# Kernel optimization log

Hardware: AMD Instinct MI355X
Metric: run time of the kernel (lower is better)

Reference implementation:

```python
import jax, jax.numpy as jnp
import numpy as np

EPS = 1e-5
B, BEAMS, DEPTH, NEXP, D = 2048, 4, 3, 4, 128

def _conv(x, w, b):
    y = jax.lax.conv_general_dilated(x, w, (1, 1), 'VALID',
                                     dimension_numbers=('NCHW', 'OIHW', 'NCHW'))
    return y + b[None, :, None, None]

def _bn(x, g, bt):
    m = jnp.mean(x, axis=(0, 2, 3), keepdims=True)
    v = jnp.var(x, axis=(0, 2, 3), keepdims=True)
    return (x - m) * jax.lax.rsqrt(v + EPS) * g[None, :, None, None] + bt[None, :, None, None]

def _pool(x):
    return jax.lax.reduce_window(x, 0.0, jax.lax.add, (1, 1, 2, 2), (1, 1, 2, 2), 'VALID') * 0.25

def setup_inputs() -> dict:
    key = jax.random.key(0)
    ks = jax.random.split(key, 16)
    s = 0.05
    return {
        'x': jax.random.normal(ks[0], (B, 1, 32, 32), jnp.float32),
        'traj': jax.random.normal(ks[1], (DEPTH, B * BEAMS, NEXP), jnp.float32),
        'score_values': jax.random.uniform(ks[2], (BEAMS, DEPTH), jnp.float32, 0.5, 1.0),
        'c1w': jax.random.normal(ks[3], (32, 1, 3, 3), jnp.float32) * s,
        'c1b': jnp.zeros((32,), jnp.float32),
        'c2w': jax.random.normal(ks[4], (32, 32, 3, 3), jnp.float32) * s,
        'c2b': jnp.zeros((32,), jnp.float32),
        'c3w': jax.random.normal(ks[5], (32, 32, 3, 3), jnp.float32) * s,
        'c3b': jnp.zeros((32,), jnp.float32),
        'g1': jnp.ones((32,), jnp.float32), 'bt1': jnp.zeros((32,), jnp.float32),
        'g2': jnp.ones((32,), jnp.float32), 'bt2': jnp.zeros((32,), jnp.float32),
        'g3': jnp.ones((32,), jnp.float32), 'bt3': jnp.zeros((32,), jnp.float32),
        'We': jax.random.normal(ks[6], (3, D, D), jnp.float32) * s,   # (expert, in, out)
        'be': jax.random.normal(ks[7], (3, D), jnp.float32) * s,
        'Wo': jax.random.normal(ks[8], (10, D), jnp.float32) * s,
        'bo': jnp.zeros((10,), jnp.float32),
    }

def reference(x, traj, score_values, c1w, c1b, c2w, c2b, c3w, c3b,
              g1, bt1, g2, bt2, g3, bt3, We, be, Wo, bo):
    h = _pool(jax.nn.relu(_bn(_conv(x, c1w, c1b), g1, bt1)))
    h = _pool(jax.nn.relu(_bn(_conv(h, c2w, c2b), g2, bt2)))
    h = _pool(jax.nn.relu(_bn(_conv(h, c3w, c3b), g3, bt3)))
    feat = h.reshape(B, -1)                                   # [B, 128]
    hs = jnp.broadcast_to(feat[:, None, :], (B, BEAMS, D)).reshape(B * BEAMS, D)
    for step in range(DEPTH):
        idx = jnp.argmax(traj[step], axis=-1)                  # [N] in 0..3
        lin = jnp.einsum('nd,edh->neh', hs, We) + be[None]     # [N, 3, 128]
        all_out = jnp.concatenate([lin, hs[:, None, :]], axis=1)  # expert 3 = Identity
        hs = jax.nn.relu(jnp.take_along_axis(all_out, idx[:, None, None], axis=1)[:, 0])
    preds = hs @ Wo.T + bo                                     # [N, 10]
    return preds * jnp.prod(score_values)
```

## Files before the change

### kernel.cpp

```cpp
#include <hip/hip_runtime.h>
#include <hip/hip_bf16.h>

#define EPSV 1e-5f
typedef __hip_bfloat16 bf16;
typedef __attribute__((ext_vector_type(8))) short v8s;
typedef __attribute__((ext_vector_type(4))) float v4f;
__device__ __forceinline__ float b2f(bf16 v) { return __bfloat162float(v); }
__device__ __forceinline__ bf16 f2b(float v) { return __float2bfloat16(v); }
__device__ __forceinline__ float bs2f(short s) {
  return __uint_as_float(((unsigned)(unsigned short)s) << 16);
}
__device__ __forceinline__ short f2bs(float v) {
  bf16 b = __float2bfloat16(v);
  return *(short*)&b;
}

__global__ __launch_bounds__(256) void fill_k(float* __restrict__ out, float val, int n)
{
  int i = blockIdx.x * 256 + threadIdx.x;
  if (i < n) out[i] = val;
}

__global__ __launch_bounds__(256) void setup_k(
    const float* __restrict__ w2, const float* __restrict__ w3,
    const float* __restrict__ We, const float* __restrict__ Wo,
    bf16* __restrict__ w2b, bf16* __restrict__ w3b,
    bf16* __restrict__ Web, bf16* __restrict__ Wob,
    int* __restrict__ cnt27, float* __restrict__ Macc,
    float* __restrict__ Sacc2, float* __restrict__ Sacc3)
{
  int i = blockIdx.x * 256 + threadIdx.x;
  if (i < 64) cnt27[i] = 0;
  if (i < 512) {
    Macc[i] = 0.f;
    Sacc2[i] = 0.f;
    Sacc3[i] = 0.f;
  }
  if (i < 9216) {
    int oc = i / 288, r = i - oc * 288, s = r >> 5, ic = r & 31;
    w2b[i] = f2b(w2[oc * 288 + ic * 9 + s]);
  } else if (i < 18432) {
    int j = i - 9216;
    int oc = j / 288, r = j - oc * 288, s = r >> 5, ic = r & 31;
    w3b[j] = f2b(w3[oc * 288 + ic * 9 + s]);
  } else if (i < 18432 + 49152) {
    Web[i - 18432] = f2b(We[i - 18432]);
  } else if (i < 18432 + 49152 + 2048) {
    int j = i - 18432 - 49152;
    int k = j >> 4, o = j & 15;
    Wob[j] = (o < 10) ? f2b(Wo[o * 128 + k]) : f2b(0.f);
  }
}

__global__ __launch_bounds__(256) void front_k(
    const float* __restrict__ traj, const float* __restrict__ x,
    int* __restrict__ cnt27, int* __restrict__ lists, float* __restrict__ Macc)
{
  int t = threadIdx.x;
  if (blockIdx.x < 32) {
    int row = blockIdx.x * 256 + t;
    __shared__ int lcnt[64], lbase[64];
    if (t < 64) lcnt[t] = 0;
    __syncthreads();
    int e[3];
#pragma unroll
    for (int s = 0; s < 3; ++s) {
      float4 tv = ((const float4*)traj)[s * 8192 + row];
      int ee = 0; float bv = tv.x;
      if (tv.y > bv) { bv = tv.y; ee = 1; }
      if (tv.z > bv) { bv = tv.z; ee = 2; }
      if (tv.w > bv) { bv = tv.w; ee = 3; }
      e[s] = ee;
    }
    int sig = e[0] + 4 * e[1] + 16 * e[2];
    int my = atomicAdd(&lcnt[sig], 1);
    __syncthreads();
    if (t < 64) lbase[t] = atomicAdd(&cnt27[t], lcnt[t]);
    __syncthreads();
    lists[sig * 8192 + lbase[sig] + my] = row;
    return;
  }
  int blk = blockIdx.x - 32;
  __shared__ __align__(16) float xs[1024];
  float M[45], S[9];
#pragma unroll
  for (int k = 0; k < 45; ++k) M[k] = 0.f;
#pragma unroll
  for (int k = 0; k < 9; ++k) S[k] = 0.f;
  for (int im = 0; im < 4; ++im) {
    int img = blk * 4 + im;
    ((float4*)xs)[t] = ((const float4*)(x + img * 1024))[t];
    __syncthreads();
    for (int p = t; p < 900; p += 256) {
      int y = p / 30, xx = p - y * 30;
      const float* r0 = xs + y * 32 + xx;
      float v[9];
      v[0] = r0[0];  v[1] = r0[1];  v[2] = r0[2];
      v[3] = r0[32]; v[4] = r0[33]; v[5] = r0[34];
      v[6] = r0[64]; v[7] = r0[65]; v[8] = r0[66];
      int idx = 0;
#pragma unroll
      for (int i = 0; i < 9; ++i) {
        S[i] += v[i];
#pragma unroll
        for (int j = i; j < 9; ++j) M[idx++] = fmaf(v[i], v[j], M[idx]);
      }
    }
    __syncthreads();
  }
  float a[54];
#pragma unroll
  for (int k = 0; k < 45; ++k) a[k] = M[k];
#pragma unroll
  for (int k = 0; k < 9; ++k) a[45 + k] = S[k];
#pragma unroll
  for (int k = 0; k < 54; ++k) {
#pragma unroll
    for (int off = 32; off; off >>= 1) a[k] += __shfl_down(a[k], off, 64);
  }
  __shared__ float red[4][54];
  int wv = t >> 6, lane = t & 63;
  if (lane == 0) {
#pragma unroll
    for (int k = 0; k < 54; ++k) red[wv][k] = a[k];
  }
  __syncthreads();
  if (t < 54)
    atomicAdd(&Macc[(blk & 7) * 64 + t], red[0][t] + red[1][t] + red[2][t] + red[3][t]);
}

__global__ __launch_bounds__(512, 4) void conv12_k(
    const float* __restrict__ x, const float* __restrict__ w1,
    const float* __restrict__ b1, const float* __restrict__ g1,
    const float* __restrict__ bt1, const float* __restrict__ Macc,
    const bf16* __restrict__ w2b, bf16* __restrict__ conv2out,
    float* __restrict__ Sacc2)
{
  int img = blockIdx.x, t = threadIdx.x;
  __shared__ __align__(16) float xs[1024];
  __shared__ float Ms[54], scs[32], shs[32];
  __shared__ short plds[225 * 40];
  __shared__ __align__(16) short w2l[32 * 296];
  __shared__ float red[8][32][2];
  if (t < 256) ((float4*)xs)[t] = ((const float4*)(x + img * 1024))[t];
  {
    const int* w2i = (const int*)w2b;
    int* w2li = (int*)w2l;
#pragma unroll
    for (int k = 0; k < 9; ++k) {
      int i = k * 512 + t;
      int row = i / 144, col = i - row * 144;
      w2li[row * 148 + col] = w2i[i];
    }
  }
  if (t >= 256 && t < 310) {
    int k = t - 256;
    float s = 0.f;
#pragma unroll
    for (int sl = 0; sl < 8; ++sl) s += Macc[sl * 64 + k];
    Ms[k] = s;
  }
  __syncthreads();
  if (t < 32) {
    float w[9];
#pragma unroll
    for (int j = 0; j < 9; ++j) w[j] = w1[t * 9 + j];
    float bias = b1[t];
    float wS = 0.f;
#pragma unroll
    for (int i = 0; i < 9; ++i) wS = fmaf(w[i], Ms[45 + i], wS);
    float wMw = 0.f;
    int idx = 0;
#pragma unroll
    for (int i = 0; i < 9; ++i)
#pragma unroll
      for (int j = i; j < 9; ++j) {
        float coef = (i == j) ? 1.f : 2.f;
        wMw = fmaf(coef * w[i] * w[j], Ms[idx], wMw);
        ++idx;
      }
    const float Np = 2048.f * 900.f;
    float mean = (wS + Np * bias) / Np;
    float sumsq = wMw + 2.f * bias * wS + Np * bias * bias;
    float var = sumsq / Np - mean * mean;
    float sc = g1[t] / sqrtf(var + EPSV);
    scs[t] = sc;
    shs[t] = bt1[t] - mean * sc;
  }
  __syncthreads();
  {
    int ch = t & 31, pg = t >> 5;
    if (pg < 15) {
      float w[9];
#pragma unroll
      for (int j = 0; j < 9; ++j) w[j] = w1[ch * 9 + j];
      float bias = b1[ch], sc = scs[ch], sh = shs[ch];
      const float* rp = xs + 2 * pg * 32;
      float2 l0 = *(const float2*)(rp);
      float2 l1 = *(const float2*)(rp + 32);
      float2 l2 = *(const float2*)(rp + 64);
      float2 l3 = *(const float2*)(rp + 96);
      float a0 = l0.x, b0 = l0.y, a1 = l1.x, b1v = l1.y;
      float a2 = l2.x, b2 = l2.y, a3 = l3.x, b3 = l3.y;
      short* orow = plds + pg * 15 * 40 + ch;
#pragma unroll
      for (int px = 0; px < 15; ++px) {
        int xb = 2 * px;
        float2 p0v = *(const float2*)(rp + xb + 2);
        float2 p1v = *(const float2*)(rp + xb + 34);
        float2 p2v = *(const float2*)(rp + xb + 66);
        float2 p3v = *(const float2*)(rp + xb + 98);
        float e0 = p0v.x, f0 = p0v.y, e1 = p1v.x, f1 = p1v.y;
        float e2 = p2v.x, f2 = p2v.y, e3 = p3v.x, f3 = p3v.y;
        float v00 = bias, v01 = bias, v10 = bias, v11 = bias;
        v00 = fmaf(a0, w[0], v00); v00 = fmaf(b0, w[1], v00); v00 = fmaf(e0, w[2], v00);
        v00 = fmaf(a1, w[3], v00); v00 = fmaf(b1v, w[4], v00); v00 = fmaf(e1, w[5], v00);
        v00 = fmaf(a2, w[6], v00); v00 = fmaf(b2, w[7], v00); v00 = fmaf(e2, w[8], v00);
        v01 = fmaf(b0, w[0], v01); v01 = fmaf(e0, w[1], v01); v01 = fmaf(f0, w[2], v01);
        v01 = fmaf(b1v, w[3], v01); v01 = fmaf(e1, w[4], v01); v01 = fmaf(f1, w[5], v01);
        v01 = fmaf(b2, w[6], v01); v01 = fmaf(e2, w[7], v01); v01 = fmaf(f2, w[8], v01);
        v10 = fmaf(a1, w[0], v10); v10 = fmaf(b1v, w[1], v10); v10 = fmaf(e1, w[2], v10);
        v10 = fmaf(a2, w[3], v10); v10 = fmaf(b2, w[4], v10); v10 = fmaf(e2, w[5], v10);
        v10 = fmaf(a3, w[6], v10); v10 = fmaf(b3, w[7], v10); v10 = fmaf(e3, w[8], v10);
        v11 = fmaf(b1v, w[0], v11); v11 = fmaf(e1, w[1], v11); v11 = fmaf(f1, w[2], v11);
        v11 = fmaf(b2, w[3], v11); v11 = fmaf(e2, w[4], v11); v11 = fmaf(f2, w[5], v11);
        v11 = fmaf(b3, w[6], v11); v11 = fmaf(e3, w[7], v11); v11 = fmaf(f3, w[8], v11);
        float r = fmaxf(fmaf(v00, sc, sh), 0.f) + fmaxf(fmaf(v01, sc, sh), 0.f)
                + fmaxf(fmaf(v10, sc, sh), 0.f) + fmaxf(fmaf(v11, sc, sh), 0.f);
        orow[px * 40] = f2bs(r * 0.25f);
        a0 = e0; a1 = e1; a2 = e2; a3 = e3;
        b0 = f0; b1v = f1; b2 = f2; b3 = f3;
      }
    }
  }
  __syncthreads();
  int lane = t & 63, wv = t >> 6;
  int m = lane & 15, kg = lane >> 4;
  const short* bp0 = w2l + m * 296 + kg * 8;
  const short* bp1 = w2l + (16 + m) * 296 + kg * 8;
  float rs0 = 0.f, rss0 = 0.f, rs1 = 0.f, rss1 = 0.f;
  for (int tile = wv; tile < 11; tile += 8) {
    int pix = tile * 16 + m;
    int cpix = pix < 169 ? pix : 168;
    int y = cpix / 13, xcol = cpix - y * 13;
    const short* ap = plds + (y * 15 + xcol) * 40 + kg * 8;
    v4f acc0 = {0.f, 0.f, 0.f, 0.f}, acc1 = {0.f, 0.f, 0.f, 0.f};
#pragma unroll
    for (int ky = 0; ky < 3; ++ky)
#pragma unroll
      for (int kx = 0; kx < 3; ++kx) {
        int s = ky * 3 + kx;
        v8s a = *(const v8s*)(ap + (ky * 15 + kx) * 40);
        v8s b0 = *(const v8s*)(bp0 + s * 32);
        v8s b1 = *(const v8s*)(bp1 + s * 32);
        acc0 = __builtin_amdgcn_mfma_f32_16x16x32_bf16(a, b0, acc0, 0, 0, 0);
        acc1 = __builtin_amdgcn_mfma_f32_16x16x32_bf16(a, b1, acc1, 0, 0, 0);
      }
#pragma unroll
    for (int j = 0; j < 4; ++j) {
      int pr = tile * 16 + kg * 4 + j;
      if (pr < 169) {
        rs0 += acc0[j]; rss0 = fmaf(acc0[j], acc0[j], rss0);
        rs1 += acc1[j]; rss1 = fmaf(acc1[j], acc1[j], rss1);
        unsigned base = (img * 169 + pr) * 32;
        conv2out[base + m] = f2b(acc0[j]);
        conv2out[base + 16 + m] = f2b(acc1[j]);
      }
    }
  }
  rs0 += __shfl_xor(rs0, 16, 64);  rss0 += __shfl_xor(rss0, 16, 64);
  rs0 += __shfl_xor(rs0, 32, 64);  rss0 += __shfl_xor(rss0, 32, 64);
  rs1 += __shfl_xor(rs1, 16, 64);  rss1 += __shfl_xor(rss1, 16, 64);
  rs1 += __shfl_xor(rs1, 32, 64);  rss1 += __shfl_xor(rss1, 32, 64);
  if (lane < 16) {
    red[wv][lane][0] = rs0;      red[wv][lane][1] = rss0;
    red[wv][16 + lane][0] = rs1; red[wv][16 + lane][1] = rss1;
  }
  __syncthreads();
  if (t < 64) {
    int cc = t >> 1, j = t & 1;
    float s = 0.f;
#pragma unroll
    for (int w8 = 0; w8 < 8; ++w8) s += red[w8][cc][j];
    atomicAdd(&Sacc2[(img & 7) * 64 + t], s);
  }
}

__global__ __launch_bounds__(256, 2) void conv3_mfma_k(
    const bf16* __restrict__ conv2out, const bf16* __restrict__ w3b,
    const float* __restrict__ Sacc2, const float* __restrict__ g2,
    const float* __restrict__ bt2, float* __restrict__ conv3out,
    float* __restrict__ Sacc3)
{
  int t = threadIdx.x, lane = t & 63, wv = t >> 6;
  int m = lane & 15, kg = lane >> 4;
  __shared__ float lsc[32], lsh[32];
  __shared__ short plds[4][36 * 40];
  __shared__ float red[4][32][2];
  if (t < 32) {
    const float invn = 1.f / (2048.f * 169.f);
    float s = 0.f, ssum = 0.f;
#pragma unroll
    for (int sl = 0; sl < 8; ++sl) {
      s += Sacc2[sl * 64 + 2 * t];
      ssum += Sacc2[sl * 64 + 2 * t + 1];
    }
    float mean = s * invn;
    float var = ssum * invn - mean * mean;
    float sc = g2[t] / sqrtf(var + EPSV);
    lsc[t] = sc;
    lsh[t] = bt2[t] - mean * sc;
  }
  __syncthreads();
  int img = blockIdx.x * 4 + wv;
#pragma unroll
  for (int k = 0; k < 18; ++k) {
    int e = k * 64 + lane;
    int pp = e >> 5, c = e & 31;
    int py = pp / 6, px = pp - py * 6;
    int ip0 = (2 * py) * 13 + 2 * px;
    const bf16* bp = conv2out + (img * 169 + ip0) * 32 + c;
    float sc = lsc[c], sh = lsh[c];
    float v = fmaxf(fmaf(b2f(bp[0]), sc, sh), 0.f)
            + fmaxf(fmaf(b2f(bp[32]), sc, sh), 0.f)
            + fmaxf(fmaf(b2f(bp[13 * 32]), sc, sh), 0.f)
            + fmaxf(fmaf(b2f(bp[14 * 32]), sc, sh), 0.f);
    plds[wv][pp * 40 + c] = f2bs(v * 0.25f);
  }
  const short* wbs = (const short*)w3b;
  v8s bfr[9][2];
#pragma unroll
  for (int s = 0; s < 9; ++s)
#pragma unroll
    for (int ob = 0; ob < 2; ++ob)
      bfr[s][ob] = *(const v8s*)(wbs + (ob * 16 + m) * 288 + s * 32 + kg * 8);

  int y = m >> 2, xcol = m & 3;
  const short* ap = plds[wv] + (y * 6 + xcol) * 40 + kg * 8;
  v4f acc0 = {0.f, 0.f, 0.f, 0.f}, acc1 = {0.f, 0.f, 0.f, 0.f};
#pragma unroll
  for (int ky = 0; ky < 3; ++ky)
#pragma unroll
    for (int kx = 0; kx < 3; ++kx) {
      v8s a = *(const v8s*)(ap + (ky * 6 + kx) * 40);
      acc0 = __builtin_amdgcn_mfma_f32_16x16x32_bf16(a, bfr[ky * 3 + kx][0], acc0, 0, 0, 0);
      acc1 = __builtin_amdgcn_mfma_f32_16x16x32_bf16(a, bfr[ky * 3 + kx][1], acc1, 0, 0, 0);
    }
  float rs0 = 0.f, rss0 = 0.f, rs1 = 0.f, rss1 = 0.f;
#pragma unroll
  for (int j = 0; j < 4; ++j) {
    rs0 += acc0[j]; rss0 = fmaf(acc0[j], acc0[j], rss0);
    rs1 += acc1[j]; rss1 = fmaf(acc1[j], acc1[j], rss1);
    int pr = kg * 4 + j;
    unsigned base = (img * 16 + pr) * 32;
    float* o = conv3out;
    o[base + m] = acc0[j];
    o[base + 16 + m] = acc1[j];
  }
  rs0 += __shfl_xor(rs0, 16, 64);  rss0 += __shfl_xor(rss0, 16, 64);
  rs0 += __shfl_xor(rs0, 32, 64);  rss0 += __shfl_xor(rss0, 32, 64);
  rs1 += __shfl_xor(rs1, 16, 64);  rss1 += __shfl_xor(rss1, 16, 64);
  rs1 += __shfl_xor(rs1, 32, 64);  rss1 += __shfl_xor(rss1, 32, 64);
  if (lane < 16) {
    red[wv][lane][0] = rs0;      red[wv][lane][1] = rss0;
    red[wv][16 + lane][0] = rs1; red[wv][16 + lane][1] = rss1;
  }
  __syncthreads();
  if (t < 64) {
    int cc = t >> 1, j = t & 1;
    atomicAdd(&Sacc3[(blockIdx.x & 7) * 64 + t],
              red[0][cc][j] + red[1][cc][j] + red[2][cc][j] + red[3][cc][j]);
  }
}

__global__ __launch_bounds__(256) void moe_fused_k(
    const float* __restrict__ conv3out, const float* __restrict__ Sacc3,
    const float* __restrict__ g3, const float* __restrict__ bt3,
    const bf16* __restrict__ Web, const float* __restrict__ be,
    const bf16* __restrict__ Wob, const float* __restrict__ bo,
    const float* __restrict__ sv, const int* __restrict__ cnt27,
    const int* __restrict__ lists, float* __restrict__ out)
{
  int t = threadIdx.x, lane = t & 63, wv = t >> 6;
  int m = lane & 15, kg = lane >> 4;
  __shared__ float st[4][16][132];
  __shared__ int scnt[64], stile[64];
  __shared__ float lsc[32], lsh[32];

  if (t < 32) {
    const float invn = 1.f / (2048.f * 16.f);
    float s = 0.f, ssum = 0.f;
#pragma unroll
    for (int sl = 0; sl < 8; ++sl) {
      s += Sacc3[sl * 64 + 2 * t];
      ssum += Sacc3[sl * 64 + 2 * t + 1];
    }
    float mean = s * invn;
    float var = ssum * invn - mean * mean;
    float sc = g3[t] / sqrtf(var + EPSV);
    lsc[t] = sc;
    lsh[t] = bt3[t] - mean * sc;
  }
  if (t >= 64 && t < 128) scnt[t - 64] = cnt27[t - 64];
  __syncthreads();
  if (t == 0) {
    int b = 0;
#pragma unroll
    for (int s = 0; s < 64; ++s) { stile[s] = b; b += (scnt[s] + 15) >> 4; }
  }
  __syncthreads();

  int g = blockIdx.x * 4 + wv;
  int sig = -1, tile = 0, cntS = 0;
#pragma unroll
  for (int s = 0; s < 64; ++s) {
    int nt = (scnt[s] + 15) >> 4;
    if (g >= stile[s] && g < stile[s] + nt) { sig = s; tile = g - stile[s]; cntS = scnt[s]; }
  }
  if (sig < 0) return;
  const int* lp = lists + sig * 8192;
  int ra = tile * 16 + m;
  int rowA = lp[ra < cntS ? ra : cntS - 1];

  {
    int img = rowA >> 2;
    const float* cbase = conv3out + img * 512 + kg * 8;
#pragma unroll
    for (int q4 = 0; q4 < 8; ++q4) {
      int c = kg * 8 + q4;
      const float* cp = cbase + q4;
      float sc = lsc[c], sh = lsh[c];
      float r[16];
#pragma unroll
      for (int p = 0; p < 16; ++p)
        r[p] = fmaxf(fmaf(cp[p * 32], sc, sh), 0.f);
      st[wv][m][kg * 32 + q4 * 4 + 0] = (r[0] + r[1] + r[4] + r[5]) * 0.25f;
      st[wv][m][kg * 32 + q4 * 4 + 1] = (r[2] + r[3] + r[6] + r[7]) * 0.25f;
      st[wv][m][kg * 32 + q4 * 4 + 2] = (r[8] + r[9] + r[12] + r[13]) * 0.25f;
      st[wv][m][kg * 32 + q4 * 4 + 3] = (r[10] + r[11] + r[14] + r[15]) * 0.25f;
    }
  }

  int es[3] = { sig & 3, (sig >> 2) & 3, sig >> 4 };
#pragma unroll
  for (int stp = 0; stp < 3; ++stp) {
    int e = es[stp];
    if (e == 3) continue;
    const short* wbs = (const short*)(Web + e * 16384);
    v8s afr[4];
#pragma unroll
    for (int kk = 0; kk < 4; ++kk) {
      float4 a0 = *(const float4*)&st[wv][m][kk * 32 + kg * 8];
      float4 a1 = *(const float4*)&st[wv][m][kk * 32 + kg * 8 + 4];
      afr[kk][0] = f2bs(a0.x); afr[kk][1] = f2bs(a0.y);
      afr[kk][2] = f2bs(a0.z); afr[kk][3] = f2bs(a0.w);
      afr[kk][4] = f2bs(a1.x); afr[kk][5] = f2bs(a1.y);
      afr[kk][6] = f2bs(a1.z); afr[kk][7] = f2bs(a1.w);
    }
#pragma unroll
    for (int ob = 0; ob < 8; ++ob) {
      v4f acc = {0.f, 0.f, 0.f, 0.f};
#pragma unroll
      for (int kk = 0; kk < 4; ++kk) {
        v8s bfr;
#pragma unroll
        for (int j = 0; j < 8; ++j)
          bfr[j] = wbs[(kk * 32 + kg * 8 + j) * 128 + ob * 16 + m];
        acc = __builtin_amdgcn_mfma_f32_16x16x32_bf16(afr[kk], bfr, acc, 0, 0, 0);
      }
      float bb = be[e * 128 + ob * 16 + m];
#pragma unroll
      for (int j = 0; j < 4; ++j)
        st[wv][kg * 4 + j][ob * 16 + m] = fmaxf(acc[j] + bb, 0.f);
    }
  }

  float ps = 1.f;
#pragma unroll
  for (int i = 0; i < 12; ++i) ps *= sv[i];
  const short* wos = (const short*)Wob;
  v8s afr[4];
#pragma unroll
  for (int kk = 0; kk < 4; ++kk) {
    float4 a0 = *(const float4*)&st[wv][m][kk * 32 + kg * 8];
    float4 a1 = *(const float4*)&st[wv][m][kk * 32 + kg * 8 + 4];
    afr[kk][0] = f2bs(a0.x); afr[kk][1] = f2bs(a0.y);
    afr[kk][2] = f2bs(a0.z); afr[kk][3] = f2bs(a0.w);
    afr[kk][4] = f2bs(a1.x); afr[kk][5] = f2bs(a1.y);
    afr[kk][6] = f2bs(a1.z); afr[kk][7] = f2bs(a1.w);
  }
  v4f acc = {0.f, 0.f, 0.f, 0.f};
#pragma unroll
  for (int kk = 0; kk < 4; ++kk) {
    v8s bfr;
#pragma unroll
    for (int j = 0; j < 8; ++j)
      bfr[j] = wos[(kk * 32 + kg * 8 + j) * 16 + m];
    acc = __builtin_amdgcn_mfma_f32_16x16x32_bf16(afr[kk], bfr, acc, 0, 0, 0);
  }
  if (m < 10) {
    float bov = bo[m];
#pragma unroll
    for (int j = 0; j < 4; ++j) {
      int idx = tile * 16 + kg * 4 + j;
      if (idx < cntS) out[lp[idx] * 10 + m] = (acc[j] + bov) * ps;
    }
  }
}

extern "C" void kernel_launch(void* const* d_in, const int* in_sizes, int n_in,
                              void* d_out, int out_size, void* d_ws, size_t ws_size,
                              hipStream_t stream)
{
  float* out = (float*)d_out;

  static const int EXP[19] = {2097152, 98304, 12, 288, 32, 9216, 32, 9216, 32,
                              32, 32, 32, 32, 32, 32, 49152, 384, 1280, 10};
  int bad = -1;
  if (n_in != 19) bad = 100;
  else
    for (int i = 0; i < 19; ++i)
      if (in_sizes[i] != EXP[i]) { bad = i; break; }
  if (bad >= 0) {
    fill_k<<<(out_size + 255) / 256, 256, 0, stream>>>(out, 1000.f + 10.f * bad, out_size);
    return;
  }
  const size_t NEED = 75771904;
  if (ws_size < NEED) {
    fill_k<<<(out_size + 255) / 256, 256, 0, stream>>>(
        out, 3000.f + (float)(ws_size >> 20), out_size);
    return;
  }

  const float* x    = (const float*)d_in[0];
  const float* traj = (const float*)d_in[1];
  const float* sv   = (const float*)d_in[2];
  const float* c1w  = (const float*)d_in[3];
  const float* c1b  = (const float*)d_in[4];
  const float* c2w  = (const float*)d_in[5];
  const float* c3w  = (const float*)d_in[7];
  const float* g1   = (const float*)d_in[9];
  const float* bt1  = (const float*)d_in[10];
  const float* g2   = (const float*)d_in[11];
  const float* bt2  = (const float*)d_in[12];
  const float* g3   = (const float*)d_in[13];
  const float* bt3  = (const float*)d_in[14];
  const float* We   = (const float*)d_in[15];
  const float* be   = (const float*)d_in[16];
  const float* Wo   = (const float*)d_in[17];
  const float* bo   = (const float*)d_in[18];

  char* w = (char*)d_ws;
  bf16*  conv2out = (bf16*)(w + 29491200);
  bf16*  Web      = (bf16*)(w + 56360960);
  float* conv3out = (float*)(w + 61079552);
  float* hsB      = (float*)(w + 69468160);
  float* Macc     = (float*)(w + 73662464);
  float* Sacc2    = (float*)(w + 73664512);
  float* Sacc3    = (float*)(w + 73666560);
  int*   cnt27    = (int*)(w + 73668608);
  bf16*  Wob      = (bf16*)(w + 73670656);
  int*   lists    = (int*)(w + 73674752);
  bf16*  w2b      = (bf16*)hsB;
  bf16*  w3b      = w2b + 9216;

  setup_k<<<272, 256, 0, stream>>>(c2w, c3w, We, Wo, w2b, w3b, Web, Wob,
                                   cnt27, Macc, Sacc2, Sacc3);
  front_k<<<544, 256, 0, stream>>>(traj, x, cnt27, lists, Macc);
  conv12_k<<<2048, 512, 0, stream>>>(x, c1w, c1b, g1, bt1, Macc, w2b, conv2out, Sacc2);
  conv3_mfma_k<<<512, 256, 0, stream>>>(conv2out, w3b, Sacc2, g2, bt2, conv3out, Sacc3);
  moe_fused_k<<<256, 256, 0, stream>>>(conv3out, Sacc3, g3, bt3, Web, be, Wob, bo,
                                       sv, cnt27, lists, out);
}
```

Measured before the change: 92.75 us.

## Warp-specialize conv12 into producer/consumer pipeline over four images per block

Each block of conv12 now processes four images instead of one, and its eight waves are split into two roles. Waves 0-3 compute conv1+BN+ReLU+pool for image i into a double-buffered LDS tile, while waves 4-7 run the MFMA conv2 on image i-1. This amortizes the per-block setup (loading w2 into LDS, computing BN1 statistics) over four images and overlaps the scalar conv1 work with the matrix-core conv2 work. In exchange, shared memory roughly doubles, the grid shrinks to 512 blocks, and each role now has half the waves available for its stage.

Result: faster. 87.42 us, median of 2 (-5.7%).

```diff
diff --git a/kernel.cpp b/kernel.cpp
--- a/kernel.cpp
+++ b/kernel.cpp
@@ -136,13 +136,13 @@
     const bf16* __restrict__ w2b, bf16* __restrict__ conv2out,
     float* __restrict__ Sacc2)
 {
-  int img = blockIdx.x, t = threadIdx.x;
-  __shared__ __align__(16) float xs[1024];
+  int t = threadIdx.x, lane = t & 63, wv = t >> 6;
+  int m = lane & 15, kg = lane >> 4;
+  __shared__ __align__(16) float xs[2][1024];
   __shared__ float Ms[54], scs[32], shs[32];
-  __shared__ short plds[225 * 40];
+  __shared__ short plds[2][225 * 40];
   __shared__ __align__(16) short w2l[32 * 296];
-  __shared__ float red[8][32][2];
-  if (t < 256) ((float4*)xs)[t] = ((const float4*)(x + img * 1024))[t];
+  __shared__ float red[4][32][2];
   {
     const int* w2i = (const int*)w2b;
     int* w2li = (int*)w2l;
@@ -153,12 +153,11 @@
       w2li[row * 148 + col] = w2i[i];
     }
   }
-  if (t >= 256 && t < 310) {
-    int k = t - 256;
+  if (t < 54) {
     float s = 0.f;
 #pragma unroll
-    for (int sl = 0; sl < 8; ++sl) s += Macc[sl * 64 + k];
-    Ms[k] = s;
+    for (int sl = 0; sl < 8; ++sl) s += Macc[sl * 64 + t];
+    Ms[t] = s;
   }
   __syncthreads();
   if (t < 32) {
@@ -188,101 +187,111 @@
     shs[t] = bt1[t] - mean * sc;
   }
   __syncthreads();
-  {
-    int ch = t & 31, pg = t >> 5;
-    if (pg < 15) {
+
+  int img0 = blockIdx.x * 4;
+  float rs0 = 0.f, rss0 = 0.f, rs1 = 0.f, rss1 = 0.f;
+
+  for (int it = 0; it <= 4; ++it) {
+    if (wv < 4 && it < 4)
+      ((float4*)xs[it & 1])[t] = ((const float4*)(x + (img0 + it) * 1024))[t];
+    __syncthreads();
+    if (wv < 4 && it < 4) {
+      int ch = t & 31, rg = t >> 5;
       float w[9];
 #pragma unroll
       for (int j = 0; j < 9; ++j) w[j] = w1[ch * 9 + j];
       float bias = b1[ch], sc = scs[ch], sh = shs[ch];
-      const float* rp = xs + 2 * pg * 32;
-      float2 l0 = *(const float2*)(rp);
-      float2 l1 = *(const float2*)(rp + 32);
-      float2 l2 = *(const float2*)(rp + 64);
-      float2 l3 = *(const float2*)(rp + 96);
-      float a0 = l0.x, b0 = l0.y, a1 = l1.x, b1v = l1.y;
-      float a2 = l2.x, b2 = l2.y, a3 = l3.x, b3 = l3.y;
-      short* orow = plds + pg * 15 * 40 + ch;
-#pragma unroll
-      for (int px = 0; px < 15; ++px) {
-        int xb = 2 * px;
-        float2 p0v = *(const float2*)(rp + xb + 2);
-        float2 p1v = *(const float2*)(rp + xb + 34);
-        float2 p2v = *(const float2*)(rp + xb + 66);
-        float2 p3v = *(const float2*)(rp + xb + 98);
-        float e0 = p0v.x, f0 = p0v.y, e1 = p1v.x, f1 = p1v.y;
-        float e2 = p2v.x, f2 = p2v.y, e3 = p3v.x, f3 = p3v.y;
-        float v00 = bias, v01 = bias, v10 = bias, v11 = bias;
-        v00 = fmaf(a0, w[0], v00); v00 = fmaf(b0, w[1], v00); v00 = fmaf(e0, w[2], v00);
-        v00 = fmaf(a1, w[3], v00); v00 = fmaf(b1v, w[4], v00); v00 = fmaf(e1, w[5], v00);
-        v00 = fmaf(a2, w[6], v00); v00 = fmaf(b2, w[7], v00); v00 = fmaf(e2, w[8], v00);
-        v01 = fmaf(b0, w[0], v01); v01 = fmaf(e0, w[1], v01); v01 = fmaf(f0, w[2], v01);
-        v01 = fmaf(b1v, w[3], v01); v01 = fmaf(e1, w[4], v01); v01 = fmaf(f1, w[5], v01);
-        v01 = fmaf(b2, w[6], v01); v01 = fmaf(e2, w[7], v01); v01 = fmaf(f2, w[8], v01);
-        v10 = fmaf(a1, w[0], v10); v10 = fmaf(b1v, w[1], v10); v10 = fmaf(e1, w[2], v10);
-        v10 = fmaf(a2, w[3], v10); v10 = fmaf(b2, w[4], v10); v10 = fmaf(e2, w[5], v10);
-        v10 = fmaf(a3, w[6], v10); v10 = fmaf(b3, w[7], v10); v10 = fmaf(e3, w[8], v10);
-        v11 = fmaf(b1v, w[0], v11); v11 = fmaf(e1, w[1], v11); v11 = fmaf(f1, w[2], v11);
-        v11 = fmaf(b2, w[3], v11); v11 = fmaf(e2, w[4], v11); v11 = fmaf(f2, w[5], v11);
-        v11 = fmaf(b3, w[6], v11); v11 = fmaf(e3, w[7], v11); v11 = fmaf(f3, w[8], v11);
-        float r = fmaxf(fmaf(v00, sc, sh), 0.f) + fmaxf(fmaf(v01, sc, sh), 0.f)
-                + fmaxf(fmaf(v10, sc, sh), 0.f) + fmaxf(fmaf(v11, sc, sh), 0.f);
-        orow[px * 40] = f2bs(r * 0.25f);
-        a0 = e0; a1 = e1; a2 = e2; a3 = e3;
-        b0 = f0; b1v = f1; b2 = f2; b3 = f3;
+      const float* xb = xs[it & 1];
+      short* pbase = plds[it & 1];
+      for (int rr = rg; rr < 15; rr += 8) {
+        const float* rp = xb + 2 * rr * 32;
+        float2 l0 = *(const float2*)(rp);
+        float2 l1 = *(const float2*)(rp + 32);
+        float2 l2 = *(const float2*)(rp + 64);
+        float2 l3 = *(const float2*)(rp + 96);
+        float a0 = l0.x, b0 = l0.y, a1 = l1.x, b1v = l1.y;
+        float a2 = l2.x, b2 = l2.y, a3 = l3.x, b3 = l3.y;
+        short* orow = pbase + rr * 15 * 40 + ch;
+#pragma unroll
+        for (int px = 0; px < 15; ++px) {
+          int xb2 = 2 * px;
+          float2 p0v = *(const float2*)(rp + xb2 + 2);
+          float2 p1v = *(const float2*)(rp + xb2 + 34);
+          float2 p2v = *(const float2*)(rp + xb2 + 66);
+          float2 p3v = *(const float2*)(rp + xb2 + 98);
+          float e0 = p0v.x, f0 = p0v.y, e1 = p1v.x, f1 = p1v.y;
+          float e2 = p2v.x, f2 = p2v.y, e3 = p3v.x, f3 = p3v.y;
+          float v00 = bias, v01 = bias, v10 = bias, v11 = bias;
+          v00 = fmaf(a0, w[0], v00); v00 = fmaf(b0, w[1], v00); v00 = fmaf(e0, w[2], v00);
+          v00 = fmaf(a1, w[3], v00); v00 = fmaf(b1v, w[4], v00); v00 = fmaf(e1, w[5], v00);
+          v00 = fmaf(a2, w[6], v00); v00 = fmaf(b2, w[7], v00); v00 = fmaf(e2, w[8], v00);
+          v01 = fmaf(b0, w[0], v01); v01 = fmaf(e0, w[1], v01); v01 = fmaf(f0, w[2], v01);
+          v01 = fmaf(b1v, w[3], v01); v01 = fmaf(e1, w[4], v01); v01 = fmaf(f1, w[5], v01);
+          v01 = fmaf(b2, w[6], v01); v01 = fmaf(e2, w[7], v01); v01 = fmaf(f2, w[8], v01);
+          v10 = fmaf(a1, w[0], v10); v10 = fmaf(b1v, w[1], v10); v10 = fmaf(e1, w[2], v10);
+          v10 = fmaf(a2, w[3], v10); v10 = fmaf(b2, w[4], v10); v10 = fmaf(e2, w[5], v10);
+          v10 = fmaf(a3, w[6], v10); v10 = fmaf(b3, w[7], v10); v10 = fmaf(e3, w[8], v10);
+          v11 = fmaf(b1v, w[0], v11); v11 = fmaf(e1, w[1], v11); v11 = fmaf(f1, w[2], v11);
+          v11 = fmaf(b2, w[3], v11); v11 = fmaf(e2, w[4], v11); v11 = fmaf(f2, w[5], v11);
+          v11 = fmaf(b3, w[6], v11); v11 = fmaf(e3, w[7], v11); v11 = fmaf(f3, w[8], v11);
+          float r = fmaxf(fmaf(v00, sc, sh), 0.f) + fmaxf(fmaf(v01, sc, sh), 0.f)
+                  + fmaxf(fmaf(v10, sc, sh), 0.f) + fmaxf(fmaf(v11, sc, sh), 0.f);
+          orow[px * 40] = f2bs(r * 0.25f);
+          a0 = e0; a1 = e1; a2 = e2; a3 = e3;
+          b0 = f0; b1v = f1; b2 = f2; b3 = f3;
+        }
       }
-    }
-  }
-  __syncthreads();
-  int lane = t & 63, wv = t >> 6;
-  int m = lane & 15, kg = lane >> 4;
-  const short* bp0 = w2l + m * 296 + kg * 8;
-  const short* bp1 = w2l + (16 + m) * 296 + kg * 8;
-  float rs0 = 0.f, rss0 = 0.f, rs1 = 0.f, rss1 = 0.f;
-  for (int tile = wv; tile < 11; tile += 8) {
-    int pix = tile * 16 + m;
-    int cpix = pix < 169 ? pix : 168;
-    int y = cpix / 13, xcol = cpix - y * 13;
-    const short* ap = plds + (y * 15 + xcol) * 40 + kg * 8;
-    v4f acc0 = {0.f, 0.f, 0.f, 0.f}, acc1 = {0.f, 0.f, 0.f, 0.f};
-#pragma unroll
-    for (int ky = 0; ky < 3; ++ky)
-#pragma unroll
-      for (int kx = 0; kx < 3; ++kx) {
-        int s = ky * 3 + kx;
-        v8s a = *(const v8s*)(ap + (ky * 15 + kx) * 40);
-        v8s b0 = *(const v8s*)(bp0 + s * 32);
-        v8s b1 = *(const v8s*)(bp1 + s * 32);
-        acc0 = __builtin_amdgcn_mfma_f32_16x16x32_bf16(a, b0, acc0, 0, 0, 0);
-        acc1 = __builtin_amdgcn_mfma_f32_16x16x32_bf16(a, b1, acc1, 0, 0, 0);
+    } else if (wv >= 4 && it > 0) {
+      int cimg = img0 + it - 1;
+      const short* pbase = plds[(it - 1) & 1];
+      const short* bp0 = w2l + m * 296 + kg * 8;
+      const short* bp1 = w2l + (16 + m) * 296 + kg * 8;
+      for (int tile = wv - 4; tile < 11; tile += 4) {
+        int pix = tile * 16 + m;
+        int cpix = pix < 169 ? pix : 168;
+        int y = cpix / 13, xcol = cpix - y * 13;
+        const short* ap = pbase + (y * 15 + xcol) * 40 + kg * 8;
+        v4f acc0 = {0.f, 0.f, 0.f, 0.f}, acc1 = {0.f, 0.f, 0.f, 0.f};
+#pragma unroll
+        for (int ky = 0; ky < 3; ++ky)
+#pragma unroll
+          for (int kx = 0; kx < 3; ++kx) {
+            int s = ky * 3 + kx;
+            v8s a = *(const v8s*)(ap + (ky * 15 + kx) * 40);
+            v8s b0 = *(const v8s*)(bp0 + s * 32);
+            v8s b1 = *(const v8s*)(bp1 + s * 32);
+            acc0 = __builtin_amdgcn_mfma_f32_16x16x32_bf16(a, b0, acc0, 0, 0, 0);
+            acc1 = __builtin_amdgcn_mfma_f32_16x16x32_bf16(a, b1, acc1, 0, 0, 0);
+          }
+#pragma unroll
+        for (int j = 0; j < 4; ++j) {
+          int pr = tile * 16 + kg * 4 + j;
+          if (pr < 169) {
+            rs0 += acc0[j]; rss0 = fmaf(acc0[j], acc0[j], rss0);
+            rs1 += acc1[j]; rss1 = fmaf(acc1[j], acc1[j], rss1);
+            unsigned base = (cimg * 169 + pr) * 32;
+            conv2out[base + m] = f2b(acc0[j]);
+            conv2out[base + 16 + m] = f2b(acc1[j]);
+          }
+        }
       }
-#pragma unroll
-    for (int j = 0; j < 4; ++j) {
-      int pr = tile * 16 + kg * 4 + j;
-      if (pr < 169) {
-        rs0 += acc0[j]; rss0 = fmaf(acc0[j], acc0[j], rss0);
-        rs1 += acc1[j]; rss1 = fmaf(acc1[j], acc1[j], rss1);
-        unsigned base = (img * 169 + pr) * 32;
-        conv2out[base + m] = f2b(acc0[j]);
-        conv2out[base + 16 + m] = f2b(acc1[j]);
-      }
-    }
-  }
+    }
+    __syncthreads();
+  }
+
   rs0 += __shfl_xor(rs0, 16, 64);  rss0 += __shfl_xor(rss0, 16, 64);
   rs0 += __shfl_xor(rs0, 32, 64);  rss0 += __shfl_xor(rss0, 32, 64);
   rs1 += __shfl_xor(rs1, 16, 64);  rss1 += __shfl_xor(rss1, 16, 64);
   rs1 += __shfl_xor(rs1, 32, 64);  rss1 += __shfl_xor(rss1, 32, 64);
-  if (lane < 16) {
-    red[wv][lane][0] = rs0;      red[wv][lane][1] = rss0;
-    red[wv][16 + lane][0] = rs1; red[wv][16 + lane][1] = rss1;
+  if (wv >= 4 && lane < 16) {
+    red[wv - 4][lane][0] = rs0;      red[wv - 4][lane][1] = rss0;
+    red[wv - 4][16 + lane][0] = rs1; red[wv - 4][16 + lane][1] = rss1;
   }
   __syncthreads();
   if (t < 64) {
     int cc = t >> 1, j = t & 1;
-    float s = 0.f;
-#pragma unroll
-    for (int w8 = 0; w8 < 8; ++w8) s += red[w8][cc][j];
-    atomicAdd(&Sacc2[(img & 7) * 64 + t], s);
+    float s = red[0][cc][j] + red[1][cc][j] + red[2][cc][j] + red[3][cc][j];
+    atomicAdd(&Sacc2[(blockIdx.x & 7) * 64 + t], s);
   }
 }
 
@@ -567,7 +576,7 @@
   setup_k<<<272, 256, 0, stream>>>(c2w, c3w, We, Wo, w2b, w3b, Web, Wob,
                                    cnt27, Macc, Sacc2, Sacc3);
   front_k<<<544, 256, 0, stream>>>(traj, x, cnt27, lists, Macc);
-  conv12_k<<<2048, 512, 0, stream>>>(x, c1w, c1b, g1, bt1, Macc, w2b, conv2out, Sacc2);
+  conv12_k<<<512, 512, 0, stream>>>(x, c1w, c1b, g1, bt1, Macc, w2b, conv2out, Sacc2);
   conv3_mfma_k<<<512, 256, 0, stream>>>(conv2out, w3b, Sacc2, g2, bt2, conv3out, Sacc3);
   moe_fused_k<<<256, 256, 0, stream>>>(conv3out, Sacc3, g3, bt3, Web, be, Wob, bo,
                                        sv, cnt27, lists, out);
```
